# Kernel optimization log

Hardware: AMD Instinct MI355X
Metric: run time of the kernel (lower is better)

Reference implementation:

```python
import jax, jax.numpy as jnp
import numpy as np

B, N, F = 32, 2048, 1024   # batch, n_stock, in_features
OUT = 1024                 # out_features
HS = 4 * N                 # sorted-MLP hidden
HF = 4 * F                 # feature-MLP hidden


def setup_inputs() -> dict:
    key = jax.random.key(0)
    ks = jax.random.split(key, 5)
    x = jax.random.normal(ks[0], (B, N, F), dtype=jnp.float32)
    # SortedDimWiseMLP params (Linear(N->HS), Linear(HS->N)); torch Linear: y = x @ W.T + b
    sw1 = jax.random.normal(ks[1], (HS, N), dtype=jnp.float32) / np.sqrt(N)   # ~orthogonal scale
    sb1 = jnp.zeros((HS,), dtype=jnp.float32)
    sw2 = jax.random.normal(ks[2], (N, HS), dtype=jnp.float32) * 0.01
    sb2 = jnp.zeros((N,), dtype=jnp.float32)
    # DimWiseMLP params (Linear(F->HF), Linear(HF->OUT))
    fw1 = jax.random.normal(ks[3], (HF, F), dtype=jnp.float32) / np.sqrt(F)
    fb1 = jnp.zeros((HF,), dtype=jnp.float32)
    fw2 = jax.random.normal(ks[4], (OUT, HF), dtype=jnp.float32) * 0.01
    fb2 = jnp.zeros((OUT,), dtype=jnp.float32)
    return {"x": x, "sw1": sw1, "sb1": sb1, "sw2": sw2, "sb2": sb2,
            "fw1": fw1, "fb1": fb1, "fw2": fw2, "fb2": fb2}


def reference(x, sw1, sb1, sw2, sb2, fw1, fb1, fw2, fb2):
    # --- SortedDimWiseMLP along n_stock (dim=0 of non-batch dims) ---
    xm = jnp.swapaxes(x, 1, 2)                 # [B, F, N]
    p = jnp.argsort(xm, axis=-1)               # argsort of values
    inv = jnp.argsort(p, axis=-1)              # inverse permutation
    # torch x.scatter(-1, argsort, x) == gather with inverse permutation
    xs = jnp.take_along_axis(xm, inv, axis=-1)
    h = jax.nn.relu(jnp.einsum('bfn,hn->bfh', xs, sw1) + sb1)   # [B, F, HS]
    y = jnp.einsum('bfh,nh->bfn', h, sw2) + sb2 + xs            # skip connection
    # torch x.scatter(-1, inverse, x) == gather with argsort
    y = jnp.take_along_axis(y, p, axis=-1)
    y = jnp.swapaxes(y, 1, 2)                  # [B, N, F]
    # --- DimWiseMLP along features (dim=1 -> movedim is identity) ---
    h2 = jax.nn.relu(jnp.einsum('bnf,hf->bnh', y, fw1) + fb1)   # [B, N, HF]
    out = jnp.einsum('bnh,oh->bno', h2, fw2) + fb2              # [B, N, OUT]
    return out
```

## Files before the change

### kernel.cpp

```cpp
#include <hip/hip_runtime.h>
#include <hip/hip_bf16.h>
#include <stdint.h>

#define B_   32
#define N_   2048
#define F_   1024
#define HS_  8192
#define HF_  4096
#define OUT_ 1024

typedef __bf16 bf16x8 __attribute__((ext_vector_type(8)));
typedef float  f32x4  __attribute__((ext_vector_type(4)));
typedef unsigned long long u64;

__device__ __forceinline__ float bf2f(unsigned short u) {
  union { unsigned int i; float f; } c; c.i = ((unsigned int)u) << 16; return c.f;
}
__device__ __forceinline__ unsigned short f2bf(float f) {
  union { float f; unsigned int i; } c; c.f = f;
  unsigned int x = c.i;
  return (unsigned short)((x + 0x7FFFu + ((x >> 16) & 1u)) >> 16);
}

__global__ __launch_bounds__(256) void f2bf_kernel(
    const float* __restrict__ in, unsigned short* __restrict__ out, int n) {
  int i = (blockIdx.x * 256 + threadIdx.x) * 8;
  if (i >= n) return;
  const float4 a = ((const float4*)(in + i))[0];
  const float4 b = ((const float4*)(in + i))[1];
  unsigned int w0 = (unsigned int)f2bf(a.x) | ((unsigned int)f2bf(a.y) << 16);
  unsigned int w1 = (unsigned int)f2bf(a.z) | ((unsigned int)f2bf(a.w) << 16);
  unsigned int w2 = (unsigned int)f2bf(b.x) | ((unsigned int)f2bf(b.y) << 16);
  unsigned int w3 = (unsigned int)f2bf(b.z) | ((unsigned int)f2bf(b.w) << 16);
  *(uint4*)(out + i) = make_uint4(w0, w1, w2, w3);
}

__global__ __launch_bounds__(256) void transpose_xk(
    const float* __restrict__ x, float* __restrict__ xm) {
  __shared__ float tile[64][65];
  const int b  = blockIdx.z;
  const int n0 = blockIdx.y * 64;
  const int f0 = blockIdx.x * 64;
  const int tx = threadIdx.x & 63;
  const int ty = threadIdx.x >> 6;
  const float* xp = x + ((size_t)b * N_ + n0) * F_ + f0;
  #pragma unroll
  for (int r = 0; r < 16; ++r) {
    int n = ty + r * 4;
    tile[tx][n] = xp[(size_t)n * F_ + tx];
  }
  __syncthreads();
  float* xmp = xm + ((size_t)b * F_ + f0) * N_ + n0;
  #pragma unroll
  for (int r = 0; r < 16; ++r) {
    int f = ty + r * 4;
    xmp[(size_t)f * N_ + tx] = tile[f][tx];
  }
}

template <int K, int J>
__device__ __forceinline__ void reg_stage_ct(u64 key[32]) {
  #pragma unroll
  for (int e = 0; e < 32; ++e) {
    if ((e & J) == 0) {
      const int f = e | J;
      const bool up = ((e & K) == 0);
      u64 a = key[e], b = key[f];
      if ((a > b) == up) { key[e] = b; key[f] = a; }
    }
  }
}

template <int J>
__device__ __forceinline__ void reg_stage_u(u64 key[32], bool up) {
  #pragma unroll
  for (int e = 0; e < 32; ++e) {
    if ((e & J) == 0) {
      const int f = e | J;
      u64 a = key[e], b = key[f];
      if ((a > b) == up) { key[e] = b; key[f] = a; }
    }
  }
}

__device__ __forceinline__ void xlane_stage(u64 key[32], int m, bool up) {
  const bool lower = ((__lane_id() & m) == 0);
  const bool keep_min = (up == lower);
  #pragma unroll
  for (int e = 0; e < 32; ++e) {
    u64 a = key[e];
    u64 b = __shfl_xor(a, m, 64);
    key[e] = ((a < b) == keep_min) ? a : b;
  }
}

__global__ __launch_bounds__(256, 4) void sort_kernel(
    const float* __restrict__ xm,
    unsigned short* __restrict__ xs,
    unsigned short* __restrict__ inv) {
  __shared__ __align__(16) unsigned int sbuf[4][N_];
  const int t    = threadIdx.x;
  const int w    = t >> 6;
  const int lane = t & 63;
  const int row  = blockIdx.x * 4 + w;
  const size_t rb = (size_t)row * N_;
  const int i0   = lane * 32;

  u64 key[32];
  unsigned int vbf[16];
  const float4* rp = (const float4*)(xm + rb + i0);
  #pragma unroll
  for (int q = 0; q < 8; ++q) {
    const float4 v = rp[q];
    vbf[2 * q]     = (unsigned int)f2bf(v.x) | ((unsigned int)f2bf(v.y) << 16);
    vbf[2 * q + 1] = (unsigned int)f2bf(v.z) | ((unsigned int)f2bf(v.w) << 16);
    const float fv[4] = {v.x, v.y, v.z, v.w};
    #pragma unroll
    for (int e = 0; e < 4; ++e) {
      union { float f; unsigned int i; } c; c.f = fv[e];
      unsigned int m = (c.i & 0x80000000u) ? ~c.i : (c.i | 0x80000000u);
      key[q * 4 + e] = (((u64)m) << 32) | (u64)(i0 + q * 4 + e);
    }
  }

  reg_stage_ct<2, 1>(key);
  reg_stage_ct<4, 2>(key);  reg_stage_ct<4, 1>(key);
  reg_stage_ct<8, 4>(key);  reg_stage_ct<8, 2>(key);  reg_stage_ct<8, 1>(key);
  reg_stage_ct<16, 8>(key); reg_stage_ct<16, 4>(key);
  reg_stage_ct<16, 2>(key); reg_stage_ct<16, 1>(key);

  #pragma unroll 1
  for (int k = 32; k <= N_; k <<= 1) {
    const bool up = ((i0 & k) == 0);
    #pragma unroll 1
    for (int m = k >> 6; m >= 1; m >>= 1)
      xlane_stage(key, m, up);
    reg_stage_u<16>(key, up);
    reg_stage_u<8>(key, up);
    reg_stage_u<4>(key, up);
    reg_stage_u<2>(key, up);
    reg_stage_u<1>(key, up);
  }

  #pragma unroll
  for (int e = 0; e < 32; ++e) {
    const unsigned int orig  = (unsigned int)key[e] & (N_ - 1);
    const unsigned int val16 = (vbf[e >> 1] >> ((e & 1) * 16)) & 0xFFFFu;
    sbuf[w][orig] = (val16 << 16) | (unsigned int)(i0 + e);
  }

  const unsigned int* sb = sbuf[w];
  unsigned int* xs32  = (unsigned int*)(xs + rb);
  unsigned int* inv32 = (unsigned int*)(inv + rb);
  #pragma unroll
  for (int q = 0; q < 8; ++q) {
    const int w0 = q * 256 + lane * 4;
    const uint4 W = *(const uint4*)(sb + w0);
    uint2 xw, iw;
    xw.x = (W.x >> 16) | (W.y & 0xFFFF0000u);
    xw.y = (W.z >> 16) | (W.w & 0xFFFF0000u);
    iw.x = (W.x & 0xFFFFu) | (W.y << 16);
    iw.y = (W.z & 0xFFFFu) | (W.w << 16);
    *(uint2*)(xs32  + (w0 >> 1)) = xw;
    *(uint2*)(inv32 + (w0 >> 1)) = iw;
  }
}

template <int EPI>
__global__ __launch_bounds__(256) void gemm_bt(
    const unsigned short* __restrict__ A,
    const unsigned short* __restrict__ Bt,
    const float* __restrict__ bias,
    const unsigned short* __restrict__ skip,
    void* __restrict__ Cv,
    int N, int K) {
  __shared__ __align__(16) unsigned short As[128 * 64];
  __shared__ __align__(16) unsigned short Bs[128 * 64];
  const int n0   = blockIdx.x * 128;
  const int m0   = blockIdx.y * 128;
  const int t    = threadIdx.x;
  const int lane = t & 63;
  const int wave = t >> 6;
  const int wm = (wave >> 1) * 64;
  const int wn = (wave & 1) * 64;
  const int lr = lane & 15;
  const int lk = (lane >> 4) * 8;

  f32x4 acc[4][4];
  #pragma unroll
  for (int i = 0; i < 4; ++i)
    #pragma unroll
    for (int j = 0; j < 4; ++j)
      acc[i][j] = (f32x4){0.f, 0.f, 0.f, 0.f};

  const unsigned short* aB = A  + (size_t)m0 * K;
  const unsigned short* bB = Bt + (size_t)n0 * K;

  for (int k0 = 0; k0 < K; k0 += 64) {
    #pragma unroll
    for (int i = 0; i < 4; ++i) {
      const int cbase = i * 256 + wave * 64;
      const int chunk = cbase + lane;
      const int row = chunk >> 3;
      const int col = (chunk & 7) << 3;
      __builtin_amdgcn_global_load_lds(
          (const __attribute__((address_space(1))) void*)(aB + (size_t)row * K + (k0 + col)),
          (__attribute__((address_space(3))) void*)(As + (size_t)cbase * 8), 16, 0, 0);
      __builtin_amdgcn_global_load_lds(
          (const __attribute__((address_space(1))) void*)(bB + (size_t)row * K + (k0 + col)),
          (__attribute__((address_space(3))) void*)(Bs + (size_t)cbase * 8), 16, 0, 0);
    }
    __syncthreads();
    #pragma unroll
    for (int kk = 0; kk < 64; kk += 32) {
      bf16x8 af[4], bv[4];
      #pragma unroll
      for (int i = 0; i < 4; ++i)
        af[i] = *(const bf16x8*)(As + (wm + i * 16 + lr) * 64 + kk + lk);
      #pragma unroll
      for (int j = 0; j < 4; ++j)
        bv[j] = *(const bf16x8*)(Bs + (wn + j * 16 + lr) * 64 + kk + lk);
      #pragma unroll
      for (int i = 0; i < 4; ++i)
        #pragma unroll
        for (int j = 0; j < 4; ++j)
          acc[i][j] = __builtin_amdgcn_mfma_f32_16x16x32_bf16(af[i], bv[j], acc[i][j], 0, 0, 0);
    }
    __syncthreads();
  }

  #pragma unroll
  for (int j = 0; j < 4; ++j) {
    const int gn = n0 + wn + j * 16 + lr;
    const float bvf = bias[gn];
    #pragma unroll
    for (int i = 0; i < 4; ++i) {
      const int gm = m0 + wm + i * 16 + (lane >> 4) * 4;
      #pragma unroll
      for (int r = 0; r < 4; ++r) {
        float v = acc[i][j][r] + bvf;
        if (EPI == 0) v = v > 0.f ? v : 0.f;
        const size_t off = (size_t)(gm + r) * N + gn;
        if (EPI == 1) v += bf2f(skip[off]);
        if (EPI == 2) ((float*)Cv)[off] = v;
        else          ((unsigned short*)Cv)[off] = f2bf(v);
      }
    }
  }
}

__global__ __launch_bounds__(256) void unpermute_kernel(
    const unsigned short* __restrict__ Y,
    const unsigned short* __restrict__ inv,
    unsigned short* __restrict__ Y2) {
  __shared__ unsigned short ot[N_][16];
  const int b  = blockIdx.x >> 6;
  const int f0 = (blockIdx.x & 63) * 16;
  const int t  = threadIdx.x;
  const size_t rbase = ((size_t)b * F_ + f0) * N_;

  for (int fl = 0; fl < 16; ++fl) {
    const uint4 yv = ((const uint4*)(Y   + rbase + (size_t)fl * N_))[t];
    const uint4 iv = ((const uint4*)(inv + rbase + (size_t)fl * N_))[t];
    unsigned int yw[4] = {yv.x, yv.y, yv.z, yv.w};
    unsigned int iw[4] = {iv.x, iv.y, iv.z, iv.w};
    #pragma unroll
    for (int e = 0; e < 8; ++e) {
      unsigned short yy = (unsigned short)(yw[e >> 1] >> ((e & 1) * 16));
      int n = (int)(unsigned short)(iw[e >> 1] >> ((e & 1) * 16));
      ot[n][(fl + (n >> 2)) & 15] = yy;
    }
  }
  __syncthreads();
  unsigned short* o = Y2 + (size_t)b * N_ * F_ + f0;
  for (int it = 0; it < 8; ++it) {
    int n = it * 256 + t;
    unsigned short tmp[16];
    #pragma unroll
    for (int fl = 0; fl < 16; ++fl) tmp[fl] = ot[n][(fl + (n >> 2)) & 15];
    unsigned int pw[8];
    #pragma unroll
    for (int q = 0; q < 8; ++q)
      pw[q] = (unsigned int)tmp[2 * q] | (((unsigned int)tmp[2 * q + 1]) << 16);
    uint4* dst = (uint4*)(o + (size_t)n * F_);
    dst[0] = make_uint4(pw[0], pw[1], pw[2], pw[3]);
    dst[1] = make_uint4(pw[4], pw[5], pw[6], pw[7]);
  }
}

extern "C" void kernel_launch(void* const* d_in, const int* in_sizes, int n_in,
                              void* d_out, int out_size, void* d_ws, size_t ws_size,
                              hipStream_t stream) {
  const float* x    = (const float*)d_in[0];
  const float* sw1f = (const float*)d_in[1];
  const float* sb1  = (const float*)d_in[2];
  const float* sw2f = (const float*)d_in[3];
  const float* sb2  = (const float*)d_in[4];
  const float* fw1f = (const float*)d_in[5];
  const float* fb1  = (const float*)d_in[6];
  const float* fw2f = (const float*)d_in[7];
  const float* fb2  = (const float*)d_in[8];
  float* outp = (float*)d_out;

  const size_t E = (size_t)B_ * F_ * N_;
  float*          xm  = (float*)d_ws;
  unsigned short* xs  = (unsigned short*)(xm + E);
  unsigned short* inv = xs + E;
  unsigned short* wb  = inv + E;
  unsigned short* wsw1 = wb;
  unsigned short* wsw2 = wsw1 + (size_t)HS_ * N_;
  unsigned short* wfw1 = wsw2 + (size_t)N_ * HS_;
  unsigned short* wfw2 = wfw1 + (size_t)HF_ * F_;
  unsigned short* Hc   = wfw2 + (size_t)OUT_ * HF_;
  unsigned short* Y    = (unsigned short*)xm;
  unsigned short* Y2   = xs;

  f2bf_kernel<<<(HS_ * N_) / 2048, 256, 0, stream>>>(sw1f, wsw1, HS_ * N_);
  f2bf_kernel<<<(N_ * HS_) / 2048, 256, 0, stream>>>(sw2f, wsw2, N_ * HS_);
  f2bf_kernel<<<(HF_ * F_) / 2048, 256, 0, stream>>>(fw1f, wfw1, HF_ * F_);
  f2bf_kernel<<<(OUT_ * HF_) / 2048, 256, 0, stream>>>(fw2f, wfw2, OUT_ * HF_);

  transpose_xk<<<dim3(F_ / 64, N_ / 64, B_), 256, 0, stream>>>(x, xm);
  sort_kernel<<<dim3(B_ * F_ / 4), 256, 0, stream>>>(xm, xs, inv);

  for (int c = 0; c < 4; ++c) {
    const size_t ro = (size_t)c * 8192;
    gemm_bt<0><<<dim3(HS_ / 128, 8192 / 128), 256, 0, stream>>>(
        xs + ro * N_, wsw1, sb1, nullptr, Hc, HS_, N_);
    gemm_bt<1><<<dim3(N_ / 128, 8192 / 128), 256, 0, stream>>>(
        Hc, wsw2, sb2, xs + ro * N_, Y + ro * N_, N_, HS_);
  }

  unpermute_kernel<<<dim3(B_ * (F_ / 16)), 256, 0, stream>>>(Y, inv, Y2);

  for (int c = 0; c < 4; ++c) {
    const size_t ro = (size_t)c * 16384;
    gemm_bt<0><<<dim3(HF_ / 128, 16384 / 128), 256, 0, stream>>>(
        Y2 + ro * F_, wfw1, fb1, nullptr, Hc, HF_, F_);
    gemm_bt<2><<<dim3(OUT_ / 128, 16384 / 128), 256, 0, stream>>>(
        Hc, wfw2, fb2, nullptr, (void*)(outp + ro * OUT_), OUT_, HF_);
  }
}
```

Before: 5.977 ms.

## Replace GEMM with 256x256 double-buffered, swizzled, 8-wave pipelined kernel

```diff
diff --git a/kernel.cpp b/kernel.cpp
--- a/kernel.cpp
+++ b/kernel.cpp
@@ -166,76 +166,160 @@
   }
 }
 
+#define GFENCE   asm volatile("" ::: "memory")
+#define BAR      __builtin_amdgcn_s_barrier()
+#define LGKM0    do { asm volatile("s_waitcnt lgkmcnt(0)" ::: "memory"); \
+                      __builtin_amdgcn_sched_barrier(0); } while (0)
+#define VMW(n)   asm volatile("s_waitcnt vmcnt(" #n ")" ::: "memory")
+
 template <int EPI>
-__global__ __launch_bounds__(256) void gemm_bt(
+__global__ __launch_bounds__(512, 2) void gemm256(
     const unsigned short* __restrict__ A,
     const unsigned short* __restrict__ Bt,
     const float* __restrict__ bias,
     const unsigned short* __restrict__ skip,
     void* __restrict__ Cv,
     int N, int K) {
-  __shared__ __align__(16) unsigned short As[128 * 64];
-  __shared__ __align__(16) unsigned short Bs[128 * 64];
-  const int n0   = blockIdx.x * 128;
-  const int m0   = blockIdx.y * 128;
+  __shared__ __align__(16) unsigned short As[2][2][256 * 32];
+  __shared__ __align__(16) unsigned short Bs[2][2][256 * 32];
+  const int n0   = blockIdx.x * 256;
+  const int m0   = blockIdx.y * 256;
   const int t    = threadIdx.x;
   const int lane = t & 63;
-  const int wave = t >> 6;
-  const int wm = (wave >> 1) * 64;
-  const int wn = (wave & 1) * 64;
-  const int lr = lane & 15;
-  const int lk = (lane >> 4) * 8;
-
-  f32x4 acc[4][4];
-  #pragma unroll
-  for (int i = 0; i < 4; ++i)
+  const int w    = t >> 6;
+  const int wr   = w >> 2;
+  const int wc   = w & 3;
+  const int lr   = lane & 15;
+  const int kg   = lane >> 4;
+
+  const int rdOff = lr * 64 + ((kg * 16) ^ (((lr >> 1) & 3) << 4));
+
+  int srow[2], scol[2];
+  #pragma unroll
+  for (int q = 0; q < 2; ++q) {
+    const int row = (w * 2 + q) * 16 + (lane >> 2);
+    const int cl  = ((lane & 3) * 16) ^ (((row >> 1) & 3) << 4);
+    srow[q] = row;
+    scol[q] = cl >> 1;
+  }
+  const unsigned short* aB = A  + (size_t)m0 * K;
+  const unsigned short* bB = Bt + (size_t)n0 * K;
+  const unsigned short* aS[2] = { aB + (size_t)srow[0] * K + scol[0],
+                                  aB + (size_t)srow[1] * K + scol[1] };
+  const unsigned short* bS[2] = { bB + (size_t)srow[0] * K + scol[0],
+                                  bB + (size_t)srow[1] * K + scol[1] };
+
+#define STAGE_U(MAT, SRC, ks, nb, k1e)                                         \
+  do {                                                                         \
+    __builtin_amdgcn_global_load_lds(                                          \
+        (const __attribute__((address_space(1))) void*)(SRC[0] + (k1e) + (ks) * 32), \
+        (__attribute__((address_space(3))) void*)(&MAT[nb][ks][0] + (w * 2 + 0) * 512), \
+        16, 0, 0);                                                             \
+    __builtin_amdgcn_global_load_lds(                                          \
+        (const __attribute__((address_space(1))) void*)(SRC[1] + (k1e) + (ks) * 32), \
+        (__attribute__((address_space(3))) void*)(&MAT[nb][ks][0] + (w * 2 + 1) * 512), \
+        16, 0, 0);                                                             \
+  } while (0)
+
+  f32x4 acc[8][4];
+  #pragma unroll
+  for (int i = 0; i < 8; ++i)
     #pragma unroll
     for (int j = 0; j < 4; ++j)
       acc[i][j] = (f32x4){0.f, 0.f, 0.f, 0.f};
 
-  const unsigned short* aB = A  + (size_t)m0 * K;
-  const unsigned short* bB = Bt + (size_t)n0 * K;
-
-  for (int k0 = 0; k0 < K; k0 += 64) {
-    #pragma unroll
-    for (int i = 0; i < 4; ++i) {
-      const int cbase = i * 256 + wave * 64;
-      const int chunk = cbase + lane;
-      const int row = chunk >> 3;
-      const int col = (chunk & 7) << 3;
-      __builtin_amdgcn_global_load_lds(
-          (const __attribute__((address_space(1))) void*)(aB + (size_t)row * K + (k0 + col)),
-          (__attribute__((address_space(3))) void*)(As + (size_t)cbase * 8), 16, 0, 0);
-      __builtin_amdgcn_global_load_lds(
-          (const __attribute__((address_space(1))) void*)(bB + (size_t)row * K + (k0 + col)),
-          (__attribute__((address_space(3))) void*)(Bs + (size_t)cbase * 8), 16, 0, 0);
-    }
-    __syncthreads();
-    #pragma unroll
-    for (int kk = 0; kk < 64; kk += 32) {
-      bf16x8 af[4], bv[4];
-      #pragma unroll
-      for (int i = 0; i < 4; ++i)
-        af[i] = *(const bf16x8*)(As + (wm + i * 16 + lr) * 64 + kk + lk);
+  const int nt = K >> 6;
+
+  STAGE_U(As, aS, 0, 0, 0);
+  STAGE_U(Bs, bS, 0, 0, 0);
+  STAGE_U(As, aS, 1, 0, 0);
+  STAGE_U(Bs, bS, 1, 0, 0);
+  VMW(4);
+  BAR;
+
+  int kt = 0;
+  #pragma unroll 1
+  for (int T = 0; T < nt; ++T, kt += 64) {
+    const int bb = T & 1;
+    const int nb = bb ^ 1;
+    const bool nl = (T + 1 < nt);
+    const int k1 = kt + 64;
+    const char* Ab0 = (const char*)(&As[bb][0][0]) + wr * 8192 + rdOff;
+    const char* Ab1 = (const char*)(&As[bb][1][0]) + wr * 8192 + rdOff;
+    const char* Bb0 = (const char*)(&Bs[bb][0][0]) + wc * 4096 + rdOff;
+    const char* Bb1 = (const char*)(&Bs[bb][1][0]) + wc * 4096 + rdOff;
+    bf16x8 aF[4], bF[4];
+
+    #pragma unroll
+    for (int j = 0; j < 4; ++j) bF[j] = *(const bf16x8*)(Bb0 + j * 1024);
+    #pragma unroll
+    for (int i = 0; i < 4; ++i) aF[i] = *(const bf16x8*)(Ab0 + i * 1024);
+    if (nl) STAGE_U(As, aS, 0, nb, k1);
+    GFENCE; BAR; LGKM0;
+    __builtin_amdgcn_s_setprio(1);
+    #pragma unroll
+    for (int i = 0; i < 4; ++i)
       #pragma unroll
       for (int j = 0; j < 4; ++j)
-        bv[j] = *(const bf16x8*)(Bs + (wn + j * 16 + lr) * 64 + kk + lk);
+        acc[i][j] = __builtin_amdgcn_mfma_f32_16x16x32_bf16(aF[i], bF[j], acc[i][j], 0, 0, 0);
+    __builtin_amdgcn_s_setprio(0);
+    __builtin_amdgcn_sched_barrier(0);
+    BAR;
+
+    #pragma unroll
+    for (int i = 0; i < 4; ++i) aF[i] = *(const bf16x8*)(Ab0 + (4 + i) * 1024);
+    if (nl) STAGE_U(Bs, bS, 0, nb, k1);
+    GFENCE; BAR; LGKM0;
+    __builtin_amdgcn_s_setprio(1);
+    #pragma unroll
+    for (int i = 0; i < 4; ++i)
       #pragma unroll
-      for (int i = 0; i < 4; ++i)
-        #pragma unroll
-        for (int j = 0; j < 4; ++j)
-          acc[i][j] = __builtin_amdgcn_mfma_f32_16x16x32_bf16(af[i], bv[j], acc[i][j], 0, 0, 0);
-    }
-    __syncthreads();
+      for (int j = 0; j < 4; ++j)
+        acc[4 + i][j] = __builtin_amdgcn_mfma_f32_16x16x32_bf16(aF[i], bF[j], acc[4 + i][j], 0, 0, 0);
+    __builtin_amdgcn_s_setprio(0);
+    __builtin_amdgcn_sched_barrier(0);
+    if (nl) { VMW(4); } else { VMW(0); }
+    BAR;
+
+    #pragma unroll
+    for (int j = 0; j < 4; ++j) bF[j] = *(const bf16x8*)(Bb1 + j * 1024);
+    #pragma unroll
+    for (int i = 0; i < 4; ++i) aF[i] = *(const bf16x8*)(Ab1 + i * 1024);
+    if (nl) STAGE_U(As, aS, 1, nb, k1);
+    GFENCE; BAR; LGKM0;
+    __builtin_amdgcn_s_setprio(1);
+    #pragma unroll
+    for (int i = 0; i < 4; ++i)
+      #pragma unroll
+      for (int j = 0; j < 4; ++j)
+        acc[i][j] = __builtin_amdgcn_mfma_f32_16x16x32_bf16(aF[i], bF[j], acc[i][j], 0, 0, 0);
+    __builtin_amdgcn_s_setprio(0);
+    __builtin_amdgcn_sched_barrier(0);
+    BAR;
+
+    #pragma unroll
+    for (int i = 0; i < 4; ++i) aF[i] = *(const bf16x8*)(Ab1 + (4 + i) * 1024);
+    if (nl) STAGE_U(Bs, bS, 1, nb, k1);
+    GFENCE; BAR; LGKM0;
+    __builtin_amdgcn_s_setprio(1);
+    #pragma unroll
+    for (int i = 0; i < 4; ++i)
+      #pragma unroll
+      for (int j = 0; j < 4; ++j)
+        acc[4 + i][j] = __builtin_amdgcn_mfma_f32_16x16x32_bf16(aF[i], bF[j], acc[4 + i][j], 0, 0, 0);
+    __builtin_amdgcn_s_setprio(0);
+    __builtin_amdgcn_sched_barrier(0);
+    if (nl) { VMW(4); } else { VMW(0); }
+    BAR;
   }
 
   #pragma unroll
   for (int j = 0; j < 4; ++j) {
-    const int gn = n0 + wn + j * 16 + lr;
+    const int gn = n0 + wc * 64 + j * 16 + lr;
     const float bvf = bias[gn];
     #pragma unroll
-    for (int i = 0; i < 4; ++i) {
-      const int gm = m0 + wm + i * 16 + (lane >> 4) * 4;
+    for (int i = 0; i < 8; ++i) {
+      const int gm = m0 + wr * 128 + i * 16 + kg * 4;
       #pragma unroll
       for (int r = 0; r < 4; ++r) {
         float v = acc[i][j][r] + bvf;
@@ -247,6 +331,7 @@
       }
     }
   }
+#undef STAGE_U
 }
 
 __global__ __launch_bounds__(256) void unpermute_kernel(
@@ -325,9 +410,9 @@
 
   for (int c = 0; c < 4; ++c) {
     const size_t ro = (size_t)c * 8192;
-    gemm_bt<0><<<dim3(HS_ / 128, 8192 / 128), 256, 0, stream>>>(
+    gemm256<0><<<dim3(HS_ / 256, 8192 / 256), 512, 0, stream>>>(
         xs + ro * N_, wsw1, sb1, nullptr, Hc, HS_, N_);
-    gemm_bt<1><<<dim3(N_ / 128, 8192 / 128), 256, 0, stream>>>(
+    gemm256<1><<<dim3(N_ / 256, 8192 / 256), 512, 0, stream>>>(
         Hc, wsw2, sb2, xs + ro * N_, Y + ro * N_, N_, HS_);
   }
 
@@ -335,9 +420,9 @@
 
   for (int c = 0; c < 4; ++c) {
     const size_t ro = (size_t)c * 16384;
-    gemm_bt<0><<<dim3(HF_ / 128, 16384 / 128), 256, 0, stream>>>(
+    gemm256<0><<<dim3(HF_ / 256, 16384 / 256), 512, 0, stream>>>(
         Y2 + ro * F_, wfw1, fb1, nullptr, Hc, HF_, F_);
-    gemm_bt<2><<<dim3(OUT_ / 128, 16384 / 128), 256, 0, stream>>>(
+    gemm256<2><<<dim3(OUT_ / 256, 16384 / 256), 512, 0, stream>>>(
         Hc, wfw2, fb2, nullptr, (void*)(outp + ro * OUT_), OUT_, HF_);
   }
 }
```

Result: faster. 5.191 ms (-13.2%).
